# Performance work log

Measured on AMD Instinct MI355X. Metric: run time of the kernel, lower is better.

Reference implementation:

```python
import jax, jax.numpy as jnp
import numpy as np

LEAK = 0.2
EPS = 1e-8


def _mod_conv(x, style, weight):
    # x: [B,C,H,W], style: [B,C], weight: [O,C,k,k]
    b, c, h, w = x.shape
    o, _, k, _ = weight.shape
    # per-sample modulation + demodulation (StyleGAN2 style)
    wmod = weight[None] * (style[:, None, :, None, None] + 1.0)  # [B,O,C,k,k]
    d = jax.lax.rsqrt(jnp.sum(wmod * wmod, axis=(2, 3, 4), keepdims=True) + EPS)
    wmod = wmod * d
    pad = (k - 1) // 2  # same padding for stride=1, dilation=1
    xg = x.reshape(1, b * c, h, w)
    wg = wmod.reshape(b * o, c, k, k)
    y = jax.lax.conv_general_dilated(
        xg, wg, window_strides=(1, 1), padding=[(pad, pad), (pad, pad)],
        dimension_numbers=('NCHW', 'OIHW', 'NCHW'), feature_group_count=b)
    return y.reshape(b, o, h, w)


def setup_inputs() -> dict:
    key = jax.random.key(0)
    ks = jax.random.split(key, 8)
    B, LAT, CIN, F, H, W = 8, 512, 256, 256, 64, 64
    K = 3
    kaiming = lambda k, shape, fan_in: jax.random.normal(k, shape, jnp.float32) * np.sqrt(2.0 / fan_in)
    return {
        'x': jax.random.normal(ks[0], (B, CIN, H, W), jnp.float32),
        'istyle': jax.random.normal(ks[1], (B, LAT), jnp.float32),
        'ws1': jax.random.normal(ks[2], (CIN, LAT), jnp.float32) * (1.0 / np.sqrt(LAT)),
        'bs1': jnp.zeros((CIN,), jnp.float32),
        'conv1_w': kaiming(ks[3], (F, CIN, K, K), CIN * K * K),
        'ws2': jax.random.normal(ks[4], (F, LAT), jnp.float32) * (1.0 / np.sqrt(LAT)),
        'bs2': jnp.zeros((F,), jnp.float32),
        'conv2_w': kaiming(ks[5], (F, F, K, K), F * K * K),
    }


def reference(x, istyle, ws1, bs1, conv1_w, ws2, bs2, conv2_w):
    b, c, h, w = x.shape
    # bilinear upsample x2, align_corners=False (half-pixel centers)
    x = jax.image.resize(x, (b, c, 2 * h, 2 * w), method='bilinear')
    s1 = istyle @ ws1.T + bs1
    x = _mod_conv(x, s1, conv1_w)
    x = jax.nn.leaky_relu(x, LEAK)
    s2 = istyle @ ws2.T + bs2
    x = _mod_conv(x, s2, conv2_w)
    return jax.nn.leaky_relu(x, LEAK)
```

## Files before the change

kernel.cpp:

```cpp
#include <hip/hip_runtime.h>

typedef __bf16 bf16x8 __attribute__((ext_vector_type(8)));
typedef float f32x4 __attribute__((ext_vector_type(4)));


#define GLDS(gsrc, ldst) __builtin_amdgcn_global_load_lds( \
    (const __attribute__((address_space(1))) unsigned int*)(gsrc), \
    (__attribute__((address_space(3))) unsigned int*)(ldst), 16, 0, 0)

#define MFMA(a, b, c) __builtin_amdgcn_mfma_f32_16x16x32_bf16((a), (b), (c), 0, 0, 0)

__global__ void style_kernel(const float* __restrict__ istyle,
                             const float* __restrict__ ws1, const float* __restrict__ bs1,
                             const float* __restrict__ ws2, const float* __restrict__ bs2,
                             float* __restrict__ sbuf) {
    int b = blockIdx.x;
    int which = blockIdx.y;
    int c = threadIdx.x;
    const float* ws = which ? ws2 : ws1;
    const float* bs = which ? bs2 : bs1;
    __shared__ float st[512];
    for (int i = threadIdx.x; i < 512; i += 256) st[i] = istyle[b * 512 + i];
    __syncthreads();
    float acc = bs[c];
    const float* wr = ws + (size_t)c * 512;
    for (int l = 0; l < 512; ++l) acc += st[l] * wr[l];
    sbuf[((size_t)which * 8 + b) * 256 + c] = acc;
}

__global__ void modw_kernel(const float* __restrict__ w, const float* __restrict__ s,
                            __bf16* __restrict__ wm) {
    int b = blockIdx.x >> 8;
    int o = blockIdx.x & 255;
    int c = threadIdx.x;
    float sm = s[(size_t)b * 256 + c] + 1.0f;
    float v[9];
    float ss = 0.f;
    const float* wr = w + ((size_t)o * 256 + c) * 9;
#pragma unroll
    for (int t = 0; t < 9; ++t) { v[t] = wr[t] * sm; ss += v[t] * v[t]; }
    __shared__ float red[256];
    red[c] = ss;
    __syncthreads();
    for (int sh = 128; sh > 0; sh >>= 1) {
        if (c < sh) red[c] += red[c + sh];
        __syncthreads();
    }
    float d = rsqrtf(red[0] + 1e-8f);
#pragma unroll
    for (int t = 0; t < 9; ++t)
        wm[(((size_t)(b * 256 + o) * 9 + t) * 256) + c] = (__bf16)(v[t] * d);
}

__global__ void zeropad_kernel(__bf16* __restrict__ xu, __bf16* __restrict__ y1) {
    int p = blockIdx.x;
    int b = blockIdx.y;
    __bf16* buf = blockIdx.z ? y1 : xu;
    int y, x;
    if (p < 130)      { y = 0;           x = p; }
    else if (p < 260) { y = 129;         x = p - 130; }
    else if (p < 388) { y = p - 260 + 1; x = 0; }
    else              { y = p - 388 + 1; x = 129; }
    uint4 z = make_uint4(0, 0, 0, 0);
    *(uint4*)(buf + (((size_t)b * 130 + y) * 130 + x) * 256 + threadIdx.x * 8) = z;
}

__global__ void upsample_kernel(const float* __restrict__ x, __bf16* __restrict__ xu) {
    int ct = blockIdx.x;
    int y  = blockIdx.y;
    int b  = blockIdx.z;
    int c0 = ct * 32;
    __shared__ float up[32 * 132];
    int tid = threadIdx.x;

    int j = y >> 1;
    int y0, y1; float wy0, wy1;
    if (y & 1) { y0 = j; y1 = (j + 1 < 64) ? j + 1 : 63; wy0 = 0.75f; wy1 = 0.25f; }
    else       { y0 = (j - 1 >= 0) ? j - 1 : 0; y1 = j; wy0 = 0.25f; wy1 = 0.75f; }

    int c  = tid >> 3;
    int xs = (tid & 7) * 16;
    const float* row0 = x + ((size_t)(b * 256 + c0 + c) * 64 + y0) * 64;
    const float* row1 = x + ((size_t)(b * 256 + c0 + c) * 64 + y1) * 64;
#pragma unroll
    for (int k = 0; k < 16; ++k) {
        int xo = xs + k;
        int i = xo >> 1;
        int x0, x1; float wx0, wx1;
        if (xo & 1) { x0 = i; x1 = (i + 1 < 64) ? i + 1 : 63; wx0 = 0.75f; wx1 = 0.25f; }
        else        { x0 = (i - 1 >= 0) ? i - 1 : 0; x1 = i; wx0 = 0.25f; wx1 = 0.75f; }
        float v0 = wx0 * row0[x0] + wx1 * row0[x1];
        float v1 = wx0 * row1[x0] + wx1 * row1[x1];
        up[c * 132 + xo] = wy0 * v0 + wy1 * v1;
    }
    __syncthreads();
    int xo = tid >> 1, half = tid & 1;
    union { __bf16 v[8]; uint4 u; } pk;
#pragma unroll
    for (int g = 0; g < 2; ++g) {
#pragma unroll
        for (int i = 0; i < 8; ++i)
            pk.v[i] = (__bf16)up[(half * 16 + g * 8 + i) * 132 + xo];
        *(uint4*)(xu + (((size_t)(b * 130) + y + 1) * 130 + xo + 1) * 256 + c0 + half * 16 + g * 8) = pk.u;
    }
}

template <int PHASE>
__global__ __launch_bounds__(512, 2) void conv_kernel(
    const __bf16* __restrict__ in,
    const __bf16* __restrict__ wmall,
    float* __restrict__ outf,
    __bf16* __restrict__ outb) {
    __shared__ __bf16 sA[2][256 * 64];
    __shared__ __bf16 sB[2][256 * 64];
    const int tid  = threadIdx.x;
    const int bid  = blockIdx.x;
    const int swz  = (bid & 7) * 64 + (bid >> 3);
    const int b    = swz >> 6;
    const int yt   = swz & 63;
    const int lane = tid & 63;
    const int wv   = tid >> 6;
    const int wo   = (wv >> 2) * 128;
    const int wn   = (wv & 3) * 64;
    const int arow = lane & 15;
    const int cgb  = lane >> 4;
    const int xA0  = (cgb ^ (arow & 7)) * 8;
    const int xA1  = xA0 ^ 32;
    const int lr   = lane >> 3;
    const int lc   = lane & 7;
    const int swz8 = (lc ^ lr) * 8;
    const __bf16* wm_b = wmall + (size_t)b * 256 * 2304;

    size_t bOff[4], aOff[4];
#pragma unroll
    for (int q = 0; q < 4; ++q) {
        int r  = q * 64 + wv * 8 + lr;
        int pr = r >> 7, px = r & 127;
        bOff[q] = ((size_t)((b * 130 + yt * 2 + pr) * 130 + px)) * 256 + swz8;
        aOff[q] = (size_t)r * 2304 + swz8;
    }

    f32x4 acc[8][4] = {};
    bf16x8 bf[4][2];

#pragma unroll
    for (int q = 0; q < 4; ++q) {
        GLDS(in + bOff[q],  &sB[0][(q * 64 + wv * 8) * 64]);
        GLDS(wm_b + aOff[q], &sA[0][(q * 64 + wv * 8) * 64]);
    }
    asm volatile("s_waitcnt vmcnt(0)" ::: "memory");
    __builtin_amdgcn_s_barrier();
    asm volatile("" ::: "memory");

    for (int t = 0; t < 36; ++t) {
        const __bf16* Ac = sA[t & 1];
        const __bf16* Bc = sB[t & 1];
        __bf16* An = sA[(t + 1) & 1];
        __bf16* Bn = sB[(t + 1) & 1];
        const bool st = (t < 35);
        const int nt = t + 1;
        const int ntap = nt >> 2, nc0 = (nt & 3) << 6;
        const int nky = ntap / 3, nkx = ntap - nky * 3;
        const size_t boff_t = (size_t)((nky * 130 + nkx) * 256 + nc0);
        const size_t aoff_t = (size_t)(ntap * 256 + nc0);

#define LOADA(qq, A00, A01, A10, A11)                                        \
        { const __bf16* ap0 = Ac + (wo + (2*(qq)) * 16 + arow) * 64;         \
          const __bf16* ap1 = Ac + (wo + (2*(qq)+1) * 16 + arow) * 64;       \
          A00 = *(const bf16x8*)(ap0 + xA0); A01 = *(const bf16x8*)(ap0 + xA1); \
          A10 = *(const bf16x8*)(ap1 + xA0); A11 = *(const bf16x8*)(ap1 + xA1); }

#define MFMAQ(M0, M1, A00, A01, A10, A11)                                    \
        _Pragma("unroll")                                                    \
        for (int j = 0; j < 4; ++j) {                                        \
            acc[M0][j] = MFMA(A00, bf[j][0], acc[M0][j]);                    \
            acc[M0][j] = MFMA(A01, bf[j][1], acc[M0][j]);                    \
            acc[M1][j] = MFMA(A10, bf[j][0], acc[M1][j]);                    \
            acc[M1][j] = MFMA(A11, bf[j][1], acc[M1][j]);                    \
        }

        {
#pragma unroll
            for (int j = 0; j < 4; ++j) {
                const __bf16* bp = Bc + (wn + j * 16 + arow) * 64;
                bf[j][0] = *(const bf16x8*)(bp + xA0);
                bf[j][1] = *(const bf16x8*)(bp + xA1);
            }
            bf16x8 a00, a01, a10, a11;
            LOADA(0, a00, a01, a10, a11);
            if (st) {
                GLDS(in + bOff[0] + boff_t, &Bn[(0 * 64 + wv * 8) * 64]);
                GLDS(in + bOff[1] + boff_t, &Bn[(1 * 64 + wv * 8) * 64]);
            }
            __builtin_amdgcn_s_barrier();
            asm volatile("" ::: "memory");
            __builtin_amdgcn_s_setprio(1);
            MFMAQ(0, 1, a00, a01, a10, a11);
            __builtin_amdgcn_s_setprio(0);
            __builtin_amdgcn_s_barrier();
            asm volatile("" ::: "memory");
        }
        {
            bf16x8 a00, a01, a10, a11;
            LOADA(1, a00, a01, a10, a11);
            if (st) {
                GLDS(in + bOff[2] + boff_t, &Bn[(2 * 64 + wv * 8) * 64]);
                GLDS(in + bOff[3] + boff_t, &Bn[(3 * 64 + wv * 8) * 64]);
            }
            __builtin_amdgcn_s_barrier();
            asm volatile("" ::: "memory");
            __builtin_amdgcn_s_setprio(1);
            MFMAQ(2, 3, a00, a01, a10, a11);
            __builtin_amdgcn_s_setprio(0);
            if (st) { asm volatile("s_waitcnt vmcnt(4)" ::: "memory"); }
            else    { asm volatile("s_waitcnt vmcnt(0)" ::: "memory"); }
            __builtin_amdgcn_s_barrier();
            asm volatile("" ::: "memory");
        }
        {
            bf16x8 a00, a01, a10, a11;
            LOADA(2, a00, a01, a10, a11);
            if (st) {
                GLDS(wm_b + aOff[0] + aoff_t, &An[(0 * 64 + wv * 8) * 64]);
                GLDS(wm_b + aOff[2] + aoff_t, &An[(2 * 64 + wv * 8) * 64]);
            }
            __builtin_amdgcn_s_barrier();
            asm volatile("" ::: "memory");
            __builtin_amdgcn_s_setprio(1);
            MFMAQ(4, 5, a00, a01, a10, a11);
            __builtin_amdgcn_s_setprio(0);
            __builtin_amdgcn_s_barrier();
            asm volatile("" ::: "memory");
        }
        {
            bf16x8 a00, a01, a10, a11;
            LOADA(3, a00, a01, a10, a11);
            if (st) {
                GLDS(wm_b + aOff[1] + aoff_t, &An[(1 * 64 + wv * 8) * 64]);
                GLDS(wm_b + aOff[3] + aoff_t, &An[(3 * 64 + wv * 8) * 64]);
            }
            __builtin_amdgcn_s_barrier();
            asm volatile("" ::: "memory");
            __builtin_amdgcn_s_setprio(1);
            MFMAQ(6, 7, a00, a01, a10, a11);
            __builtin_amdgcn_s_setprio(0);
            if (st) { asm volatile("s_waitcnt vmcnt(2)" ::: "memory"); }
            __builtin_amdgcn_s_barrier();
            asm volatile("" ::: "memory");
        }
#undef LOADA
#undef MFMAQ
    }

#pragma unroll
    for (int m = 0; m < 8; ++m) {
#pragma unroll
        for (int j = 0; j < 4; ++j) {
            int o_base = wo + m * 16 + (lane >> 4) * 4;
            int n      = wn + j * 16 + (lane & 15);
            int pr = n >> 7, px = n & 127;
            if (PHASE == 1) {
                union { __bf16 v[4]; uint2 u; } pk;
#pragma unroll
                for (int r = 0; r < 4; ++r) {
                    float v = acc[m][j][r];
                    pk.v[r] = (__bf16)((v > 0.f) ? v : 0.2f * v);
                }
                *(uint2*)(outb + (((size_t)(b * 130) + yt * 2 + pr + 1) * 130 + px + 1) * 256 + o_base) = pk.u;
            } else {
#pragma unroll
                for (int r = 0; r < 4; ++r) {
                    float v = acc[m][j][r];
                    v = (v > 0.f) ? v : 0.2f * v;
                    outf[((size_t)(b * 256 + o_base + r) * 128 + yt * 2 + pr) * 128 + px] = v;
                }
            }
        }
    }
}

extern "C" void kernel_launch(void* const* d_in, const int* in_sizes, int n_in,
                              void* d_out, int out_size, void* d_ws, size_t ws_size,
                              hipStream_t stream) {
    const float* x      = (const float*)d_in[0];
    const float* istyle = (const float*)d_in[1];
    const float* ws1    = (const float*)d_in[2];
    const float* bs1    = (const float*)d_in[3];
    const float* w1     = (const float*)d_in[4];
    const float* ws2    = (const float*)d_in[5];
    const float* bs2    = (const float*)d_in[6];
    const float* w2     = (const float*)d_in[7];
    float* out = (float*)d_out;

    char* ws = (char*)d_ws;
    __bf16* xu_p = (__bf16*)(ws);
    __bf16* y1_p = (__bf16*)(ws + 69222400);
    __bf16* wm   = (__bf16*)(ws + 138444800);
    float*  sbuf = (float*)(ws + 147881984);

    style_kernel<<<dim3(8, 2), 256, 0, stream>>>(istyle, ws1, bs1, ws2, bs2, sbuf);
    zeropad_kernel<<<dim3(516, 8, 2), 32, 0, stream>>>(xu_p, y1_p);
    upsample_kernel<<<dim3(8, 128, 8), 256, 0, stream>>>(x, xu_p);
    modw_kernel<<<dim3(2048), 256, 0, stream>>>(w1, sbuf, wm);
    conv_kernel<1><<<dim3(512), 512, 0, stream>>>(xu_p, wm, nullptr, y1_p);
    modw_kernel<<<dim3(2048), 256, 0, stream>>>(w2, sbuf + 2048, wm);
    conv_kernel<2><<<dim3(512), 512, 0, stream>>>(y1_p, wm, out, nullptr);
}
```

Before: 397.7 us.

## Stage phase-1 conv epilogue through LDS, reorder K loop, batch zero-padding

The phase-1 conv epilogue now writes its bf16 activations into a swizzled LDS tile. Each wave then writes whole 512-byte channel rows with 16-byte stores, replacing scattered 8-byte stores. The K loop order changes to channel-block-major with taps inner, which alters the global address pattern of successive loads. The zero-pad kernel packs 8 border pixels per 256-thread block, cutting its launch block count. The extra LDS round trip and syncthreads add some epilogue cost.

```diff
diff --git a/kernel.cpp b/kernel.cpp
--- a/kernel.cpp
+++ b/kernel.cpp
@@ -53,16 +53,19 @@
 }
 
 __global__ void zeropad_kernel(__bf16* __restrict__ xu, __bf16* __restrict__ y1) {
-    int p = blockIdx.x;
-    int b = blockIdx.y;
+    int p0 = blockIdx.x * 8;
+    int b  = blockIdx.y;
     __bf16* buf = blockIdx.z ? y1 : xu;
+    int p = p0 + (threadIdx.x >> 5);
+    if (p >= 516) return;
+    int chunk = threadIdx.x & 31;
     int y, x;
     if (p < 130)      { y = 0;           x = p; }
     else if (p < 260) { y = 129;         x = p - 130; }
     else if (p < 388) { y = p - 260 + 1; x = 0; }
     else              { y = p - 388 + 1; x = 129; }
     uint4 z = make_uint4(0, 0, 0, 0);
-    *(uint4*)(buf + (((size_t)b * 130 + y) * 130 + x) * 256 + threadIdx.x * 8) = z;
+    *(uint4*)(buf + (((size_t)b * 130 + y) * 130 + x) * 256 + chunk * 8) = z;
 }
 
 __global__ void upsample_kernel(const float* __restrict__ x, __bf16* __restrict__ xu) {
@@ -111,8 +114,9 @@
     const __bf16* __restrict__ wmall,
     float* __restrict__ outf,
     __bf16* __restrict__ outb) {
-    __shared__ __bf16 sA[2][256 * 64];
-    __shared__ __bf16 sB[2][256 * 64];
+    __shared__ __attribute__((aligned(128))) char smem[131072];
+    __bf16* const sA0 = (__bf16*)smem;
+    __bf16* const sB0 = (__bf16*)(smem + 65536);
     const int tid  = threadIdx.x;
     const int bid  = blockIdx.x;
     const int swz  = (bid & 7) * 64 + (bid >> 3);
@@ -145,22 +149,24 @@
 
 #pragma unroll
     for (int q = 0; q < 4; ++q) {
-        GLDS(in + bOff[q],  &sB[0][(q * 64 + wv * 8) * 64]);
-        GLDS(wm_b + aOff[q], &sA[0][(q * 64 + wv * 8) * 64]);
+        GLDS(in + bOff[q],   sB0 + (q * 64 + wv * 8) * 64);
+        GLDS(wm_b + aOff[q], sA0 + (q * 64 + wv * 8) * 64);
     }
     asm volatile("s_waitcnt vmcnt(0)" ::: "memory");
     __builtin_amdgcn_s_barrier();
     asm volatile("" ::: "memory");
 
     for (int t = 0; t < 36; ++t) {
-        const __bf16* Ac = sA[t & 1];
-        const __bf16* Bc = sB[t & 1];
-        __bf16* An = sA[(t + 1) & 1];
-        __bf16* Bn = sB[(t + 1) & 1];
+        const __bf16* Ac = sA0 + (t & 1) * 16384;
+        const __bf16* Bc = sB0 + (t & 1) * 16384;
+        __bf16* An = sA0 + ((t + 1) & 1) * 16384;
+        __bf16* Bn = sB0 + ((t + 1) & 1) * 16384;
         const bool st = (t < 35);
-        const int nt = t + 1;
-        const int ntap = nt >> 2, nc0 = (nt & 3) << 6;
-        const int nky = ntap / 3, nkx = ntap - nky * 3;
+        const int nt   = t + 1;
+        const int ncb  = nt / 9;
+        const int ntap = nt - 9 * ncb;
+        const int nc0  = ncb * 64;
+        const int nky  = ntap / 3, nkx = ntap - 3 * nky;
         const size_t boff_t = (size_t)((nky * 130 + nkx) * 256 + nc0);
         const size_t aoff_t = (size_t)(ntap * 256 + nc0);
 
@@ -189,8 +195,8 @@
             bf16x8 a00, a01, a10, a11;
             LOADA(0, a00, a01, a10, a11);
             if (st) {
-                GLDS(in + bOff[0] + boff_t, &Bn[(0 * 64 + wv * 8) * 64]);
-                GLDS(in + bOff[1] + boff_t, &Bn[(1 * 64 + wv * 8) * 64]);
+                GLDS(in + bOff[0] + boff_t, Bn + (0 * 64 + wv * 8) * 64);
+                GLDS(in + bOff[1] + boff_t, Bn + (1 * 64 + wv * 8) * 64);
             }
             __builtin_amdgcn_s_barrier();
             asm volatile("" ::: "memory");
@@ -204,8 +210,8 @@
             bf16x8 a00, a01, a10, a11;
             LOADA(1, a00, a01, a10, a11);
             if (st) {
-                GLDS(in + bOff[2] + boff_t, &Bn[(2 * 64 + wv * 8) * 64]);
-                GLDS(in + bOff[3] + boff_t, &Bn[(3 * 64 + wv * 8) * 64]);
+                GLDS(in + bOff[2] + boff_t, Bn + (2 * 64 + wv * 8) * 64);
+                GLDS(in + bOff[3] + boff_t, Bn + (3 * 64 + wv * 8) * 64);
             }
             __builtin_amdgcn_s_barrier();
             asm volatile("" ::: "memory");
@@ -221,8 +227,8 @@
             bf16x8 a00, a01, a10, a11;
             LOADA(2, a00, a01, a10, a11);
             if (st) {
-                GLDS(wm_b + aOff[0] + aoff_t, &An[(0 * 64 + wv * 8) * 64]);
-                GLDS(wm_b + aOff[2] + aoff_t, &An[(2 * 64 + wv * 8) * 64]);
+                GLDS(wm_b + aOff[0] + aoff_t, An + (0 * 64 + wv * 8) * 64);
+                GLDS(wm_b + aOff[2] + aoff_t, An + (2 * 64 + wv * 8) * 64);
             }
             __builtin_amdgcn_s_barrier();
             asm volatile("" ::: "memory");
@@ -236,8 +242,8 @@
             bf16x8 a00, a01, a10, a11;
             LOADA(3, a00, a01, a10, a11);
             if (st) {
-                GLDS(wm_b + aOff[1] + aoff_t, &An[(1 * 64 + wv * 8) * 64]);
-                GLDS(wm_b + aOff[3] + aoff_t, &An[(3 * 64 + wv * 8) * 64]);
+                GLDS(wm_b + aOff[1] + aoff_t, An + (1 * 64 + wv * 8) * 64);
+                GLDS(wm_b + aOff[3] + aoff_t, An + (3 * 64 + wv * 8) * 64);
             }
             __builtin_amdgcn_s_barrier();
             asm volatile("" ::: "memory");
@@ -252,22 +258,46 @@
 #undef MFMAQ
     }
 
-#pragma unroll
-    for (int m = 0; m < 8; ++m) {
-#pragma unroll
-        for (int j = 0; j < 4; ++j) {
-            int o_base = wo + m * 16 + (lane >> 4) * 4;
-            int n      = wn + j * 16 + (lane & 15);
-            int pr = n >> 7, px = n & 127;
-            if (PHASE == 1) {
+    __builtin_amdgcn_sched_barrier(0);
+    __syncthreads();
+
+    if (PHASE == 1) {
+        __bf16* const ot = (__bf16*)smem;
+        const int al = lane & 15;
+        const int cg = lane >> 4;
+#pragma unroll
+        for (int m = 0; m < 8; ++m) {
+#pragma unroll
+            for (int j = 0; j < 4; ++j) {
+                int n   = wn + j * 16 + al;
+                int och = wo + m * 16 + cg * 4;
                 union { __bf16 v[4]; uint2 u; } pk;
 #pragma unroll
                 for (int r = 0; r < 4; ++r) {
                     float v = acc[m][j][r];
                     pk.v[r] = (__bf16)((v > 0.f) ? v : 0.2f * v);
                 }
-                *(uint2*)(outb + (((size_t)(b * 130) + yt * 2 + pr + 1) * 130 + px + 1) * 256 + o_base) = pk.u;
-            } else {
+                *(uint2*)((char*)ot + n * 512 + ((och * 2) ^ ((n & 7) << 4))) = pk.u;
+            }
+        }
+        __syncthreads();
+        const int half = lane >> 5;
+        const int l32  = lane & 31;
+#pragma unroll
+        for (int p = 0; p < 16; ++p) {
+            int n  = wv * 32 + p * 2 + half;
+            int pr = n >> 7, px = n & 127;
+            uint4 v = *(const uint4*)((const char*)ot + n * 512 + ((l32 * 16) ^ ((n & 7) << 4)));
+            *(uint4*)(outb + (((size_t)(b * 130) + yt * 2 + pr + 1) * 130 + px + 1) * 256 + l32 * 8) = v;
+        }
+    } else {
+#pragma unroll
+        for (int m = 0; m < 8; ++m) {
+#pragma unroll
+            for (int j = 0; j < 4; ++j) {
+                int o_base = wo + m * 16 + (lane >> 4) * 4;
+                int n      = wn + j * 16 + (lane & 15);
+                int pr = n >> 7, px = n & 127;
 #pragma unroll
                 for (int r = 0; r < 4; ++r) {
                     float v = acc[m][j][r];
@@ -299,7 +329,7 @@
     float*  sbuf = (float*)(ws + 147881984);
 
     style_kernel<<<dim3(8, 2), 256, 0, stream>>>(istyle, ws1, bs1, ws2, bs2, sbuf);
-    zeropad_kernel<<<dim3(516, 8, 2), 32, 0, stream>>>(xu_p, y1_p);
+    zeropad_kernel<<<dim3(65, 8, 2), 256, 0, stream>>>(xu_p, y1_p);
     upsample_kernel<<<dim3(8, 128, 8), 256, 0, stream>>>(x, xu_p);
     modw_kernel<<<dim3(2048), 256, 0, stream>>>(w1, sbuf, wm);
     conv_kernel<1><<<dim3(512), 512, 0, stream>>>(xu_p, wm, nullptr, y1_p);
```

Result: faster. 379.5 us (-4.6%).
